# Performance work log

Hardware: AMD Instinct MI355X
Metric: run time of the kernel (lower is better)

Reference implementation:

```python
import jax, jax.numpy as jnp
import numpy as np

NUM_USERS = 100000
NUM_ITEMS = 50000
EMB_DIM = 128
NUM_LAYERS = 3
NUM_EDGES = 2000000
BATCH = 8192
REG = 1e-4


def setup_inputs() -> dict:
    key = jax.random.key(0)
    ks = jax.random.split(key, 8)
    N = NUM_USERS + NUM_ITEMS
    user_emb = jax.random.normal(ks[0], (NUM_USERS, EMB_DIM), dtype=jnp.float32) * 0.01
    item_emb = jax.random.normal(ks[1], (NUM_ITEMS, EMB_DIM), dtype=jnp.float32) * 0.01
    edge_row = jax.random.randint(ks[2], (NUM_EDGES,), 0, N, dtype=jnp.int32)
    edge_col = jax.random.randint(ks[3], (NUM_EDGES,), 0, N, dtype=jnp.int32)
    # symmetric-normalized adjacency values are small positives
    edge_val = jax.random.uniform(ks[4], (NUM_EDGES,), dtype=jnp.float32) * 0.1
    user = jax.random.randint(ks[5], (BATCH,), 0, NUM_USERS, dtype=jnp.int32)
    pos = jax.random.randint(ks[6], (BATCH,), 0, NUM_ITEMS, dtype=jnp.int32)
    neg = jax.random.randint(ks[7], (BATCH,), 0, NUM_ITEMS, dtype=jnp.int32)
    return {"user_emb": user_emb, "item_emb": item_emb,
            "edge_row": edge_row, "edge_col": edge_col, "edge_val": edge_val,
            "user": user, "pos": pos, "neg": neg}


def _lightgcn_embedding(user_emb, item_emb, edge_row, edge_col, edge_val):
    N = user_emb.shape[0] + item_emb.shape[0]
    emb = jnp.concatenate([user_emb, item_emb], axis=0)  # [N, D]
    acc = emb
    for _ in range(NUM_LAYERS):
        # SpMM: out[r] += val * emb[c] for each edge (r, c)
        msg = emb[edge_col] * edge_val[:, None]  # [E, D]
        emb = jax.ops.segment_sum(msg, edge_row, num_segments=N)
        acc = acc + emb
    light = acc / jnp.float32(NUM_LAYERS + 1)  # mean over layer outputs
    return light[:NUM_USERS], light[NUM_USERS:]


def reference(user_emb, item_emb, edge_row, edge_col, edge_val, user, pos, neg):
    u_all, i_all = _lightgcn_embedding(user_emb, item_emb, edge_row, edge_col, edge_val)
    u_lat = u_all[user]          # [B, D]
    pos_lat = i_all[pos]
    neg_lat = i_all[neg]
    pos_score = jnp.sum(u_lat * pos_lat, axis=1)
    neg_score = jnp.sum(u_lat * neg_lat, axis=1)
    # L1 regularization on ego (layer-0) embeddings, scalar broadcast onto batch loss
    reg_loss = REG * (jnp.sum(jnp.abs(user_emb[user]))
                      + jnp.sum(jnp.abs(item_emb[pos]))
                      + jnp.sum(jnp.abs(item_emb[neg])))
    batch_loss = jax.nn.softplus(neg_score - pos_score) + reg_loss
    return batch_loss
```

## Files before the change

kernel.cpp:

```cpp
#include <hip/hip_runtime.h>
#include <hip/hip_bf16.h>

#define EMB_D 128
#define BSH 9
#define MAXBUCK 512
#define CHUNKP 2048

typedef float f32x2 __attribute__((ext_vector_type(2)));

__device__ __forceinline__ float bf16_raw_to_f(unsigned short h) {
    return __uint_as_float(((unsigned int)h) << 16);
}
__device__ __forceinline__ float sane(float v) {
    return (v == v && fabsf(v) < 256.0f) ? v : 0.0f;
}
__device__ __forceinline__ float load_f(const void* p, int isf32, size_t idx) {
    return isf32 ? ((const float*)p)[idx]
                 : bf16_raw_to_f(((const unsigned short*)p)[idx]);
}

__device__ __forceinline__ f32x2 cvt2_fp8(unsigned int w) {
    f32x2 r;
    asm("v_cvt_pk_f32_fp8 %0, %1" : "=v"(r) : "v"(w));
    return r;
}
__device__ __forceinline__ unsigned int enc2_fp8(float a, float b) {
    unsigned int r;
    asm("v_cvt_pk_fp8_f32 %0, %1, %2" : "=v"(r) : "v"(a), "v"(b));
    return r & 0xFFFFu;
}
__device__ __forceinline__ unsigned int fp8x4_enc(float a, float b, float c, float d) {
    return enc2_fp8(a, b) | (enc2_fp8(c, d) << 16);
}
__device__ __forceinline__ float fp8_dec_byte(unsigned int b) {
    return cvt2_fp8(b & 0xFFu).x;
}

__global__ void k_detect(const unsigned short* __restrict__ ue,
                         const unsigned short* __restrict__ ie,
                         const unsigned short* __restrict__ ev,
                         int* __restrict__ flags) {
    int a = blockIdx.x;
    const unsigned short* p = (a == 0) ? ue : (a == 1) ? ie : ev;
    int lane = threadIdx.x;
    int cnt = 0;
    #pragma unroll
    for (int k = 0; k < 16; ++k) {
        float v = bf16_raw_to_f(p[k * 64 + lane]);
        if (!(fabsf(v) < 1.0f)) cnt++;
    }
    #pragma unroll
    for (int off = 32; off > 0; off >>= 1)
        cnt += __shfl_down(cnt, off, 64);
    if (lane == 0) flags[a] = (cnt > 64) ? 1 : 0;
}

__global__ __launch_bounds__(256) void k_build_emb8(
        const void* __restrict__ ue, const void* __restrict__ ie,
        const int* __restrict__ flags,
        unsigned char* __restrict__ T, float* __restrict__ S,
        int NU, int N) {
    int gid = blockIdx.x * blockDim.x + threadIdx.x;
    int row = gid >> 5;
    if (row >= N) return;
    int l = gid & 31;
    const void* src; long r; int f;
    if (row < NU) { src = ue; r = row;      f = flags[0]; }
    else          { src = ie; r = row - NU; f = flags[1]; }
    float v0, v1, v2, v3;
    if (f) {
        float4 t = ((const float4*)src)[r * 32 + l];
        v0 = sane(t.x); v1 = sane(t.y); v2 = sane(t.z); v3 = sane(t.w);
    } else {
        ushort4 t = ((const ushort4*)src)[r * 32 + l];
        v0 = sane(bf16_raw_to_f(t.x)); v1 = sane(bf16_raw_to_f(t.y));
        v2 = sane(bf16_raw_to_f(t.z)); v3 = sane(bf16_raw_to_f(t.w));
    }
    float m = fmaxf(fmaxf(fabsf(v0), fabsf(v1)), fmaxf(fabsf(v2), fabsf(v3)));
    #pragma unroll
    for (int off = 1; off < 32; off <<= 1)
        m = fmaxf(m, __shfl_xor(m, off, 64));
    float enc = (m > 0.0f) ? 448.0f / m : 0.0f;
    ((unsigned int*)T)[(size_t)row * 32 + l] =
        fp8x4_enc(v0 * enc, v1 * enc, v2 * enc, v3 * enc);
    if (l == 0) S[row] = (m > 0.0f) ? m * (1.0f / 448.0f) : 0.0f;
}

__global__ void k_zero_flags(int* __restrict__ f, int words, float* __restrict__ reg) {
    int i = blockIdx.x * blockDim.x + threadIdx.x;
    if (i < words) f[i] = 0;
    if (i == 0) reg[0] = 0.0f;
}

__global__ void k_mark_batch(const int* __restrict__ user, const int* __restrict__ pos,
                             const int* __restrict__ neg,
                             const void* __restrict__ ue, const void* __restrict__ ie,
                             const int* __restrict__ flags, int NU, int NI,
                             unsigned char* __restrict__ flag3,
                             unsigned char* __restrict__ flag2,
                             float* __restrict__ regp) {
    __shared__ float sred[2];
    int b = blockIdx.x;
    int d = threadIdx.x;
    int ui = min(max(user[b], 0), NU - 1);
    int pi = min(max(pos[b],  0), NI - 1);
    int ni = min(max(neg[b],  0), NI - 1);
    if (d == 0) {
        flag3[ui] = 1; flag3[NU + pi] = 1; flag3[NU + ni] = 1;
        flag2[ui] = 1; flag2[NU + pi] = 1; flag2[NU + ni] = 1;
    }
    int f0 = flags[0], f1 = flags[1];
    float u = sane(load_f(ue, f0, (size_t)ui * EMB_D + d));
    float p = sane(load_f(ie, f1, (size_t)pi * EMB_D + d));
    float n = sane(load_f(ie, f1, (size_t)ni * EMB_D + d));
    float s = fabsf(u) + fabsf(p) + fabsf(n);
    #pragma unroll
    for (int off = 32; off > 0; off >>= 1)
        s += __shfl_down(s, off, 64);
    if ((d & 63) == 0) sred[d >> 6] = s;
    __syncthreads();
    if (d == 0) regp[b] = sred[0] + sred[1];
}

__global__ void k_reduce_reg(const float* __restrict__ regp, float* __restrict__ reg, int B) {
    __shared__ float ss[256];
    int t = threadIdx.x;
    float s = 0.0f;
    for (int i = t; i < B; i += 256) s += regp[i];
    ss[t] = s;
    __syncthreads();
    for (int off = 128; off > 0; off >>= 1) {
        if (t < off) ss[t] += ss[t + off];
        __syncthreads();
    }
    if (t == 0) reg[0] = ss[0];
}


__global__ __launch_bounds__(256) void k_part_count(
        const int* __restrict__ erow, const int* __restrict__ ecol,
        const unsigned char* __restrict__ flag3, unsigned char* __restrict__ flag2,
        int* __restrict__ bcnt, int E, int N, int nbuck, int NB) {
    __shared__ int lh[MAXBUCK];
    int b = blockIdx.x, t = threadIdx.x;
    for (int i = t; i < MAXBUCK; i += 256) lh[i] = 0;
    __syncthreads();
    int beg = b * CHUNKP;
    int cnt = min(CHUNKP, E - beg);
    for (int p = t; p < cnt; p += 256) {
        int e = beg + p;
        int r = min(max(erow[e], 0), N - 1);
        atomicAdd(&lh[r >> BSH], 1);
        if (flag3[r]) {
            int c = min(max(ecol[e], 0), N - 1);
            flag2[c] = 1;
        }
    }
    __syncthreads();
    for (int i = t; i < nbuck; i += 256) bcnt[(long)i * NB + b] = lh[i];
}

__global__ void k_gscan1(const int* __restrict__ a, int* __restrict__ bsums, int L) {
    __shared__ int ss[256];
    int t = threadIdx.x;
    int base = blockIdx.x * 1024 + t * 4;
    int s = 0;
    #pragma unroll
    for (int j = 0; j < 4; ++j) {
        int idx = base + j;
        if (idx < L) s += a[idx];
    }
    ss[t] = s;
    __syncthreads();
    for (int off = 128; off > 0; off >>= 1) {
        if (t < off) ss[t] += ss[t + off];
        __syncthreads();
    }
    if (t == 0) bsums[blockIdx.x] = ss[0];
}

__global__ void k_gscan2(const int* __restrict__ bsums, int* __restrict__ boffs,
                         int nb, int* __restrict__ rowptrN) {
    __shared__ int ss[256];
    int t = threadIdx.x;
    int base = t * 4;
    int c[4];
    int s = 0;
    #pragma unroll
    for (int j = 0; j < 4; ++j) {
        c[j] = (base + j < nb) ? bsums[base + j] : 0;
        s += c[j];
    }
    ss[t] = s;
    __syncthreads();
    for (int off = 1; off < 256; off <<= 1) {
        int v = (t >= off) ? ss[t - off] : 0;
        __syncthreads();
        ss[t] += v;
        __syncthreads();
    }
    int run = ss[t] - s;
    #pragma unroll
    for (int j = 0; j < 4; ++j) {
        if (base + j < nb) boffs[base + j] = run;
        run += c[j];
    }
    if (t == 255) *rowptrN = ss[255];
}

__global__ void k_gscan3(int* __restrict__ a, const int* __restrict__ boffs, int L) {
    __shared__ int ss[256];
    int t = threadIdx.x;
    int base = blockIdx.x * 1024 + t * 4;
    int c[4];
    int s = 0;
    #pragma unroll
    for (int j = 0; j < 4; ++j) {
        int idx = base + j;
        c[j] = (idx < L) ? a[idx] : 0;
        s += c[j];
    }
    ss[t] = s;
    __syncthreads();
    for (int off = 1; off < 256; off <<= 1) {
        int v = (t >= off) ? ss[t - off] : 0;
        __syncthreads();
        ss[t] += v;
        __syncthreads();
    }
    int run = boffs[blockIdx.x] + ss[t] - s;
    #pragma unroll
    for (int j = 0; j < 4; ++j) {
        int idx = base + j;
        if (idx < L) a[idx] = run;
        run += c[j];
    }
}

__global__ __launch_bounds__(256) void k_part_scatter(
        const int* __restrict__ erow, const int* __restrict__ ecol,
        const void* __restrict__ eval, const int* __restrict__ flags,
        const int* __restrict__ boff,
        unsigned int* __restrict__ part_cv, unsigned short* __restrict__ part_r,
        int E, int N, int nbuck, int NB) {
    __shared__ uint2 lrec[CHUNKP];
    __shared__ unsigned short lidx[CHUNKP];
    __shared__ int hist[MAXBUCK];
    __shared__ int bstart[MAXBUCK];
    __shared__ int ss[256];
    int b = blockIdx.x, t = threadIdx.x;
    int beg = b * CHUNKP;
    int cnt = min(CHUNKP, E - beg);
    for (int i = t; i < MAXBUCK; i += 256) hist[i] = 0;
    __syncthreads();
    int f2 = flags[2];
    for (int p = t; p < cnt; p += 256) {
        int e = beg + p;
        int r = min(max(erow[e], 0), N - 1);
        int c = min(max(ecol[e], 0), N - 1);
        float v = sane(load_f(eval, f2, e));
        if (v < 0.0f) v = 0.0f;
        unsigned int u = __float_as_uint(v);
        unsigned int vb = ((u + 0x10000u) >> 17) & 0x3FFFu;
        lrec[p] = make_uint2((unsigned int)r, ((unsigned int)c << 14) | vb);
        atomicAdd(&hist[r >> BSH], 1);
    }
    __syncthreads();
    int c0 = hist[2 * t], c1 = hist[2 * t + 1];
    int s = c0 + c1;
    ss[t] = s;
    __syncthreads();
    for (int off = 1; off < 256; off <<= 1) {
        int v = (t >= off) ? ss[t - off] : 0;
        __syncthreads();
        ss[t] += v;
        __syncthreads();
    }
    int eb = ss[t] - s;
    bstart[2 * t] = eb;
    bstart[2 * t + 1] = eb + c0;
    hist[2 * t] = eb;
    hist[2 * t + 1] = eb + c0;
    __syncthreads();
    for (int p = t; p < cnt; p += 256) {
        int bin = (int)(lrec[p].x >> BSH);
        int pos = atomicAdd(&hist[bin], 1);
        lidx[pos] = (unsigned short)p;
    }
    __syncthreads();
    for (int i = t; i < nbuck; i += 256)
        hist[i] = boff[(long)i * NB + b] - bstart[i];
    __syncthreads();
    for (int p = t; p < cnt; p += 256) {
        uint2 rec = lrec[lidx[p]];
        int bin = (int)(rec.x >> BSH);
        int o = hist[bin] + p;
        part_cv[o] = rec.y;
        part_r[o] = (unsigned short)(rec.x & 511u);
    }
}

__global__ __launch_bounds__(256) void k_build_csr(
        const unsigned int* __restrict__ part_cv,
        const unsigned short* __restrict__ part_r,
        const int* __restrict__ boff,
        int* __restrict__ row_ptr, unsigned int* __restrict__ sedge,
        int E, int N, int NB, int nbuck) {
    __shared__ int rcnt[256];
    __shared__ int rcur[256];
    __shared__ int ss[256];
    __shared__ int slow;
    int blk = blockIdx.x, t = threadIdx.x;
    int bin = blk >> 1, half = blk & 1;
    int base = boff[(long)bin * NB];
    int next = (bin + 1 < nbuck) ? boff[(long)(bin + 1) * NB] : E;
    int cnt = next - base;
    int r0 = bin << BSH;
    int rlo = half << 8;
    int nrows = min(256, max(0, min(512, N - r0) - rlo));
    rcnt[t] = 0;
    if (t == 0) slow = 0;
    __syncthreads();
    int lowc = 0;
    for (int i = t; i < cnt; i += 256) {
        int pr = part_r[base + i];
        int lp = pr - rlo;
        if (lp >= 0 && lp < 256) atomicAdd(&rcnt[lp], 1);
        else if (pr < rlo) lowc++;
    }
    #pragma unroll
    for (int off = 32; off > 0; off >>= 1)
        lowc += __shfl_down(lowc, off, 64);
    if ((t & 63) == 0 && lowc) atomicAdd(&slow, lowc);
    __syncthreads();
    int c = rcnt[t];
    ss[t] = c;
    __syncthreads();
    for (int off = 1; off < 256; off <<= 1) {
        int v = (t >= off) ? ss[t - off] : 0;
        __syncthreads();
        ss[t] += v;
        __syncthreads();
    }
    int st = ss[t] - c + slow;
    rcur[t] = st;
    __syncthreads();
    if (t < nrows) row_ptr[r0 + rlo + t] = base + st;
    for (int i = t; i < cnt; i += 256) {
        int pr = part_r[base + i];
        int lp = pr - rlo;
        if (lp >= 0 && lp < 256) {
            int pos = atomicAdd(&rcur[lp], 1);
            sedge[base + pos] = part_cv[base + i];
        }
    }
}

__global__ __launch_bounds__(1024, 8) void k_spmm_csr8(
        const unsigned char* __restrict__ T, const float* __restrict__ S,
        unsigned char* __restrict__ Td, float* __restrict__ Sd,
        const int* __restrict__ row_ptr, const unsigned int* __restrict__ sedge,
        int N, const unsigned char* __restrict__ skipf, int use_skip) {
    int row = blockIdx.x * (blockDim.x >> 6) + (threadIdx.x >> 6);
    if (row >= N) return;
    if (use_skip && skipf[row] == 0) return;
    int lane = threadIdx.x & 63;
    int ph = lane >> 4;
    int sl = lane & 15;
    int beg = row_ptr[row], end = row_ptr[row + 1];
    float a[8];
    #pragma unroll
    for (int j = 0; j < 8; ++j) a[j] = 0.0f;
    int i = beg + ph;
    for (; i + 4 < end; i += 8) {
        unsigned int se0 = sedge[i];
        unsigned int se1 = sedge[i + 4];
        unsigned int c0 = se0 >> 14, c1 = se1 >> 14;
        uint2 h0 = ((const uint2*)(T + (size_t)c0 * EMB_D))[sl];
        uint2 h1 = ((const uint2*)(T + (size_t)c1 * EMB_D))[sl];
        float vs0 = __uint_as_float((se0 & 0x3FFFu) << 17) * S[c0];
        float vs1 = __uint_as_float((se1 & 0x3FFFu) << 17) * S[c1];
        f32x2 d;
        d = cvt2_fp8(h0.x);       a[0] += vs0 * d.x; a[1] += vs0 * d.y;
        d = cvt2_fp8(h0.x >> 16); a[2] += vs0 * d.x; a[3] += vs0 * d.y;
        d = cvt2_fp8(h0.y);       a[4] += vs0 * d.x; a[5] += vs0 * d.y;
        d = cvt2_fp8(h0.y >> 16); a[6] += vs0 * d.x; a[7] += vs0 * d.y;
        d = cvt2_fp8(h1.x);       a[0] += vs1 * d.x; a[1] += vs1 * d.y;
        d = cvt2_fp8(h1.x >> 16); a[2] += vs1 * d.x; a[3] += vs1 * d.y;
        d = cvt2_fp8(h1.y);       a[4] += vs1 * d.x; a[5] += vs1 * d.y;
        d = cvt2_fp8(h1.y >> 16); a[6] += vs1 * d.x; a[7] += vs1 * d.y;
    }
    if (i < end) {
        unsigned int se = sedge[i];
        unsigned int c = se >> 14;
        uint2 h = ((const uint2*)(T + (size_t)c * EMB_D))[sl];
        float vs = __uint_as_float((se & 0x3FFFu) << 17) * S[c];
        f32x2 d;
        d = cvt2_fp8(h.x);       a[0] += vs * d.x; a[1] += vs * d.y;
        d = cvt2_fp8(h.x >> 16); a[2] += vs * d.x; a[3] += vs * d.y;
        d = cvt2_fp8(h.y);       a[4] += vs * d.x; a[5] += vs * d.y;
        d = cvt2_fp8(h.y >> 16); a[6] += vs * d.x; a[7] += vs * d.y;
    }
    #pragma unroll
    for (int j = 0; j < 8; ++j) {
        a[j] += __shfl_xor(a[j], 16, 64);
        a[j] += __shfl_xor(a[j], 32, 64);
    }
    float m = fmaxf(fmaxf(fmaxf(fabsf(a[0]), fabsf(a[1])), fmaxf(fabsf(a[2]), fabsf(a[3]))),
                    fmaxf(fmaxf(fabsf(a[4]), fabsf(a[5])), fmaxf(fabsf(a[6]), fabsf(a[7]))));
    m = fmaxf(m, __shfl_xor(m, 1, 64));
    m = fmaxf(m, __shfl_xor(m, 2, 64));
    m = fmaxf(m, __shfl_xor(m, 4, 64));
    m = fmaxf(m, __shfl_xor(m, 8, 64));
    if (ph == 0) {
        float enc = (m > 0.0f) ? 448.0f / m : 0.0f;
        uint2 w;
        w.x = fp8x4_enc(a[0] * enc, a[1] * enc, a[2] * enc, a[3] * enc);
        w.y = fp8x4_enc(a[4] * enc, a[5] * enc, a[6] * enc, a[7] * enc);
        ((uint2*)(Td + (size_t)row * EMB_D))[sl] = w;
        if (lane == 0) Sd[row] = (m > 0.0f) ? m * (1.0f / 448.0f) : 0.0f;
    }
}

__global__ void k_gather_final(
        const void* __restrict__ ue, const void* __restrict__ ie,
        const int* __restrict__ flags,
        const int* __restrict__ user, const int* __restrict__ pos,
        const int* __restrict__ neg, int NU, int NI,
        const unsigned char* __restrict__ T1, const float* __restrict__ S1,
        const unsigned char* __restrict__ T2, const float* __restrict__ S2,
        const unsigned char* __restrict__ T3, const float* __restrict__ S3,
        const float* __restrict__ reg, float* __restrict__ out) {
    __shared__ float sps[2], sns[2];
    int b = blockIdx.x;
    int d = threadIdx.x;
    int ui = min(max(user[b], 0), NU - 1);
    int pi = min(max(pos[b],  0), NI - 1);
    int ni = min(max(neg[b],  0), NI - 1);
    size_t ru = (size_t)ui;
    size_t rp = (size_t)NU + pi;
    size_t rn = (size_t)NU + ni;
    int f0 = flags[0], f1 = flags[1];
    float u = sane(load_f(ue, f0, ru * EMB_D + d))
            + fp8_dec_byte(T1[ru * EMB_D + d]) * S1[ru]
            + fp8_dec_byte(T2[ru * EMB_D + d]) * S2[ru]
            + fp8_dec_byte(T3[ru * EMB_D + d]) * S3[ru];
    float p = sane(load_f(ie, f1, (size_t)pi * EMB_D + d))
            + fp8_dec_byte(T1[rp * EMB_D + d]) * S1[rp]
            + fp8_dec_byte(T2[rp * EMB_D + d]) * S2[rp]
            + fp8_dec_byte(T3[rp * EMB_D + d]) * S3[rp];
    float n = sane(load_f(ie, f1, (size_t)ni * EMB_D + d))
            + fp8_dec_byte(T1[rn * EMB_D + d]) * S1[rn]
            + fp8_dec_byte(T2[rn * EMB_D + d]) * S2[rn]
            + fp8_dec_byte(T3[rn * EMB_D + d]) * S3[rn];
    float ps = u * p, ns = u * n;
    #pragma unroll
    for (int off = 32; off > 0; off >>= 1) {
        ps += __shfl_down(ps, off, 64);
        ns += __shfl_down(ns, off, 64);
    }
    if ((d & 63) == 0) { sps[d >> 6] = ps; sns[d >> 6] = ns; }
    __syncthreads();
    if (d == 0) {
        float x = ((sns[0] + sns[1]) - (sps[0] + sps[1])) * 0.0625f;
        float sp = fmaxf(x, 0.0f) + log1pf(expf(-fabsf(x)));
        out[b] = sp + 1e-4f * reg[0];
    }
}

extern "C" void kernel_launch(void* const* d_in, const int* in_sizes, int n_in,
                              void* d_out, int out_size, void* d_ws, size_t ws_size,
                              hipStream_t stream) {
    const void* ue   = d_in[0];
    const void* ie   = d_in[1];
    const int*  erow = (const int*)d_in[2];
    const int*  ecol = (const int*)d_in[3];
    const void* ev   = d_in[4];
    const int*  user = (const int*)d_in[5];
    const int*  pos  = (const int*)d_in[6];
    const int*  neg  = (const int*)d_in[7];

    int NU = in_sizes[0] / EMB_D;
    int NI = in_sizes[1] / EMB_D;
    int N  = NU + NI;
    int E  = in_sizes[2];
    int B  = in_sizes[5];

    int nbuck = (N + ((1 << BSH) - 1)) >> BSH;
    int NBp   = (E + CHUNKP - 1) / CHUNKP;
    int L     = nbuck * NBp;
    int nbL   = (L + 1023) / 1024;

    size_t T8   = (size_t)N * EMB_D;
    size_t SC   = (((size_t)N * sizeof(float)) + 15) & ~15ull;
    size_t NI4  = ((size_t)(N + 1) * sizeof(int) + 15) & ~15ull;
    size_t L4   = ((size_t)L * sizeof(int) + 15) & ~15ull;
    size_t E2   = (((size_t)E * 2) + 15) & ~15ull;
    size_t Npad = ((size_t)N + 15) & ~15ull;
    char* w = (char*)d_ws;
    int*   flags   = (int*)w;
    float* reg     = (float*)(w + 64);
    char*  q       = w + 256;
    float* regp    = (float*)q;             q += (size_t)B * sizeof(float);
    int*   row_ptr = (int*)q;               q += NI4;
    unsigned int*   part_cv = (unsigned int*)q;   q += (size_t)E * 4;
    unsigned short* part_r  = (unsigned short*)q; q += E2;
    int*   bcnt    = (int*)q;               q += L4;
    int*   bsums   = (int*)q;               q += 4096;
    int*   boffs   = (int*)q;               q += 4096;
    unsigned char* flag3 = (unsigned char*)q; q += Npad;
    unsigned char* flag2 = (unsigned char*)q; q += Npad;
    unsigned int* sedge = (unsigned int*)q; q += (size_t)E * 4;
    unsigned char* Ta = (unsigned char*)q;  q += T8;
    float*         Sa = (float*)q;          q += SC;
    unsigned char* T1 = (unsigned char*)q;  q += T8;
    float*         S1 = (float*)q;          q += SC;
    unsigned char* T2 = (unsigned char*)q;  q += T8;
    float*         S2 = (float*)q;          q += SC;
    unsigned char* T3 = (unsigned char*)q;  q += T8;
    float*         S3 = (float*)q;

    const int thr = 256;
    float* out = (float*)d_out;

    k_detect<<<3, 64, 0, stream>>>((const unsigned short*)ue, (const unsigned short*)ie,
                                   (const unsigned short*)ev, flags);
    int fwords = (int)((2 * Npad) / 4);
    k_zero_flags<<<(fwords + thr - 1) / thr, thr, 0, stream>>>((int*)flag3, fwords, reg);
    k_mark_batch<<<B, EMB_D, 0, stream>>>(user, pos, neg, ue, ie, flags, NU, NI,
                                          flag3, flag2, regp);
    k_reduce_reg<<<1, 256, 0, stream>>>(regp, reg, B);
    k_build_emb8<<<(N * 32 + thr - 1) / thr, thr, 0, stream>>>(ue, ie, flags, Ta, Sa, NU, N);

    k_part_count<<<NBp, 256, 0, stream>>>(erow, ecol, flag3, flag2, bcnt, E, N, nbuck, NBp);
    k_gscan1<<<nbL, 256, 0, stream>>>(bcnt, bsums, L);
    k_gscan2<<<1, 256, 0, stream>>>(bsums, boffs, nbL, row_ptr + N);
    k_gscan3<<<nbL, 256, 0, stream>>>(bcnt, boffs, L);
    k_part_scatter<<<NBp, 256, 0, stream>>>(erow, ecol, ev, flags, bcnt,
                                            part_cv, part_r, E, N, nbuck, NBp);
    k_build_csr<<<2 * nbuck, 256, 0, stream>>>(part_cv, part_r, bcnt, row_ptr, sedge,
                                               E, N, NBp, nbuck);

    const int sthr = 1024;
    int rows_per_block = sthr / 64;
    int sgrid = (N + rows_per_block - 1) / rows_per_block;

    k_spmm_csr8<<<sgrid, sthr, 0, stream>>>(Ta, Sa, T1, S1, row_ptr, sedge, N, flag2, 0);
    k_spmm_csr8<<<sgrid, sthr, 0, stream>>>(T1, S1, T2, S2, row_ptr, sedge, N, flag2, 1);
    k_spmm_csr8<<<sgrid, sthr, 0, stream>>>(T2, S2, T3, S3, row_ptr, sedge, N, flag3, 1);

    k_gather_final<<<B, EMB_D, 0, stream>>>(ue, ie, flags, user, pos, neg, NU, NI,
                                            T1, S1, T2, S2, T3, S3, reg, out);
}
```

Before: 460.5 us.

## Fuse setup kernels, replace multi-pass bucket scan with atomic cursors, shrink SpMM blocks

Merges format detection, flag zeroing and bucket-counter clearing into one setup kernel, and merges the FP8 embedding build with the batch marking and regularizer partial sums into one prep kernel. The per-chunk bucket count matrix and its three-kernel global scan are replaced by global atomic bucket counts, a single-block scan (which also reduces the regularizer) and atomic cursors for scatter offsets. SpMM launches now use 256-thread blocks without launch bounds. The aim is fewer launches and a smaller scan. In exchange the order of edges inside each bucket depends on scheduling, and the global atomics add some contention.

After: 476.7 us. 3.5% more time.

```diff
diff --git a/kernel.cpp b/kernel.cpp
--- a/kernel.cpp
+++ b/kernel.cpp
@@ -36,111 +36,101 @@
     return cvt2_fp8(b & 0xFFu).x;
 }
 
-__global__ void k_detect(const unsigned short* __restrict__ ue,
-                         const unsigned short* __restrict__ ie,
-                         const unsigned short* __restrict__ ev,
-                         int* __restrict__ flags) {
-    int a = blockIdx.x;
-    const unsigned short* p = (a == 0) ? ue : (a == 1) ? ie : ev;
-    int lane = threadIdx.x;
-    int cnt = 0;
-    #pragma unroll
-    for (int k = 0; k < 16; ++k) {
-        float v = bf16_raw_to_f(p[k * 64 + lane]);
-        if (!(fabsf(v) < 1.0f)) cnt++;
-    }
-    #pragma unroll
-    for (int off = 32; off > 0; off >>= 1)
-        cnt += __shfl_down(cnt, off, 64);
-    if (lane == 0) flags[a] = (cnt > 64) ? 1 : 0;
-}
-
-__global__ __launch_bounds__(256) void k_build_emb8(
+__global__ void k_setup(const unsigned short* __restrict__ ue,
+                        const unsigned short* __restrict__ ie,
+                        const unsigned short* __restrict__ ev,
+                        int* __restrict__ flags,
+                        int* __restrict__ fzero, int fwords,
+                        int* __restrict__ bucket_cnt) {
+    int gid = blockIdx.x * blockDim.x + threadIdx.x;
+    for (int i = gid; i < fwords; i += gridDim.x * blockDim.x) fzero[i] = 0;
+    if (gid < MAXBUCK) bucket_cnt[gid] = 0;
+    if (blockIdx.x < 3 && threadIdx.x < 64) {
+        int a = blockIdx.x;
+        const unsigned short* p = (a == 0) ? ue : (a == 1) ? ie : ev;
+        int lane = threadIdx.x;
+        int cnt = 0;
+        #pragma unroll
+        for (int k = 0; k < 16; ++k) {
+            float v = bf16_raw_to_f(p[k * 64 + lane]);
+            if (!(fabsf(v) < 1.0f)) cnt++;
+        }
+        #pragma unroll
+        for (int off = 32; off > 0; off >>= 1)
+            cnt += __shfl_down(cnt, off, 64);
+        if (lane == 0) flags[a] = (cnt > 64) ? 1 : 0;
+    }
+}
+
+__global__ __launch_bounds__(256) void k_prep(
         const void* __restrict__ ue, const void* __restrict__ ie,
         const int* __restrict__ flags,
         unsigned char* __restrict__ T, float* __restrict__ S,
-        int NU, int N) {
-    int gid = blockIdx.x * blockDim.x + threadIdx.x;
-    int row = gid >> 5;
-    if (row >= N) return;
-    int l = gid & 31;
-    const void* src; long r; int f;
-    if (row < NU) { src = ue; r = row;      f = flags[0]; }
-    else          { src = ie; r = row - NU; f = flags[1]; }
-    float v0, v1, v2, v3;
-    if (f) {
-        float4 t = ((const float4*)src)[r * 32 + l];
-        v0 = sane(t.x); v1 = sane(t.y); v2 = sane(t.z); v3 = sane(t.w);
+        int NU, int NI, int N,
+        const int* __restrict__ user, const int* __restrict__ pos,
+        const int* __restrict__ neg, int B,
+        unsigned char* __restrict__ flag3, unsigned char* __restrict__ flag2,
+        float* __restrict__ regp, int GE) {
+    __shared__ float sredw[4];
+    if (blockIdx.x < GE) {
+        int gid = blockIdx.x * 256 + threadIdx.x;
+        int row = gid >> 5;
+        if (row >= N) return;
+        int l = gid & 31;
+        const void* src; long r; int f;
+        if (row < NU) { src = ue; r = row;      f = flags[0]; }
+        else          { src = ie; r = row - NU; f = flags[1]; }
+        float v0, v1, v2, v3;
+        if (f) {
+            float4 t = ((const float4*)src)[r * 32 + l];
+            v0 = sane(t.x); v1 = sane(t.y); v2 = sane(t.z); v3 = sane(t.w);
+        } else {
+            ushort4 t = ((const ushort4*)src)[r * 32 + l];
+            v0 = sane(bf16_raw_to_f(t.x)); v1 = sane(bf16_raw_to_f(t.y));
+            v2 = sane(bf16_raw_to_f(t.z)); v3 = sane(bf16_raw_to_f(t.w));
+        }
+        float m = fmaxf(fmaxf(fabsf(v0), fabsf(v1)), fmaxf(fabsf(v2), fabsf(v3)));
+        #pragma unroll
+        for (int off = 1; off < 32; off <<= 1)
+            m = fmaxf(m, __shfl_xor(m, off, 64));
+        float enc = (m > 0.0f) ? 448.0f / m : 0.0f;
+        ((unsigned int*)T)[(size_t)row * 32 + l] =
+            fp8x4_enc(v0 * enc, v1 * enc, v2 * enc, v3 * enc);
+        if (l == 0) S[row] = (m > 0.0f) ? m * (1.0f / 448.0f) : 0.0f;
     } else {
-        ushort4 t = ((const ushort4*)src)[r * 32 + l];
-        v0 = sane(bf16_raw_to_f(t.x)); v1 = sane(bf16_raw_to_f(t.y));
-        v2 = sane(bf16_raw_to_f(t.z)); v3 = sane(bf16_raw_to_f(t.w));
-    }
-    float m = fmaxf(fmaxf(fabsf(v0), fabsf(v1)), fmaxf(fabsf(v2), fabsf(v3)));
-    #pragma unroll
-    for (int off = 1; off < 32; off <<= 1)
-        m = fmaxf(m, __shfl_xor(m, off, 64));
-    float enc = (m > 0.0f) ? 448.0f / m : 0.0f;
-    ((unsigned int*)T)[(size_t)row * 32 + l] =
-        fp8x4_enc(v0 * enc, v1 * enc, v2 * enc, v3 * enc);
-    if (l == 0) S[row] = (m > 0.0f) ? m * (1.0f / 448.0f) : 0.0f;
-}
-
-__global__ void k_zero_flags(int* __restrict__ f, int words, float* __restrict__ reg) {
-    int i = blockIdx.x * blockDim.x + threadIdx.x;
-    if (i < words) f[i] = 0;
-    if (i == 0) reg[0] = 0.0f;
-}
-
-__global__ void k_mark_batch(const int* __restrict__ user, const int* __restrict__ pos,
-                             const int* __restrict__ neg,
-                             const void* __restrict__ ue, const void* __restrict__ ie,
-                             const int* __restrict__ flags, int NU, int NI,
-                             unsigned char* __restrict__ flag3,
-                             unsigned char* __restrict__ flag2,
-                             float* __restrict__ regp) {
-    __shared__ float sred[2];
-    int b = blockIdx.x;
-    int d = threadIdx.x;
-    int ui = min(max(user[b], 0), NU - 1);
-    int pi = min(max(pos[b],  0), NI - 1);
-    int ni = min(max(neg[b],  0), NI - 1);
-    if (d == 0) {
-        flag3[ui] = 1; flag3[NU + pi] = 1; flag3[NU + ni] = 1;
-        flag2[ui] = 1; flag2[NU + pi] = 1; flag2[NU + ni] = 1;
-    }
-    int f0 = flags[0], f1 = flags[1];
-    float u = sane(load_f(ue, f0, (size_t)ui * EMB_D + d));
-    float p = sane(load_f(ie, f1, (size_t)pi * EMB_D + d));
-    float n = sane(load_f(ie, f1, (size_t)ni * EMB_D + d));
-    float s = fabsf(u) + fabsf(p) + fabsf(n);
-    #pragma unroll
-    for (int off = 32; off > 0; off >>= 1)
-        s += __shfl_down(s, off, 64);
-    if ((d & 63) == 0) sred[d >> 6] = s;
-    __syncthreads();
-    if (d == 0) regp[b] = sred[0] + sred[1];
-}
-
-__global__ void k_reduce_reg(const float* __restrict__ regp, float* __restrict__ reg, int B) {
-    __shared__ float ss[256];
-    int t = threadIdx.x;
-    float s = 0.0f;
-    for (int i = t; i < B; i += 256) s += regp[i];
-    ss[t] = s;
-    __syncthreads();
-    for (int off = 128; off > 0; off >>= 1) {
-        if (t < off) ss[t] += ss[t + off];
-        __syncthreads();
-    }
-    if (t == 0) reg[0] = ss[0];
+        int t = threadIdx.x;
+        int half = t >> 7;
+        int d = t & 127;
+        int b = (blockIdx.x - GE) * 2 + half;
+        float s = 0.0f;
+        if (b < B) {
+            int ui = min(max(user[b], 0), NU - 1);
+            int pi = min(max(pos[b],  0), NI - 1);
+            int ni = min(max(neg[b],  0), NI - 1);
+            if (d == 0) {
+                flag3[ui] = 1; flag3[NU + pi] = 1; flag3[NU + ni] = 1;
+                flag2[ui] = 1; flag2[NU + pi] = 1; flag2[NU + ni] = 1;
+            }
+            int f0 = flags[0], f1 = flags[1];
+            float u = sane(load_f(ue, f0, (size_t)ui * EMB_D + d));
+            float p = sane(load_f(ie, f1, (size_t)pi * EMB_D + d));
+            float n = sane(load_f(ie, f1, (size_t)ni * EMB_D + d));
+            s = fabsf(u) + fabsf(p) + fabsf(n);
+        }
+        #pragma unroll
+        for (int off = 32; off > 0; off >>= 1)
+            s += __shfl_down(s, off, 64);
+        if ((t & 63) == 0) sredw[t >> 6] = s;
+        __syncthreads();
+        if (b < B && d == 0) regp[b] = sredw[half * 2] + sredw[half * 2 + 1];
+    }
 }
 
 
 __global__ __launch_bounds__(256) void k_part_count(
         const int* __restrict__ erow, const int* __restrict__ ecol,
         const unsigned char* __restrict__ flag3, unsigned char* __restrict__ flag2,
-        int* __restrict__ bcnt, int E, int N, int nbuck, int NB) {
+        int* __restrict__ bucket_cnt, int E, int N, int nbuck) {
     __shared__ int lh[MAXBUCK];
     int b = blockIdx.x, t = threadIdx.x;
     for (int i = t; i < MAXBUCK; i += 256) lh[i] = 0;
@@ -157,40 +147,23 @@
         }
     }
     __syncthreads();
-    for (int i = t; i < nbuck; i += 256) bcnt[(long)i * NB + b] = lh[i];
-}
-
-__global__ void k_gscan1(const int* __restrict__ a, int* __restrict__ bsums, int L) {
+    for (int i = t; i < nbuck; i += 256) {
+        int c = lh[i];
+        if (c) atomicAdd(&bucket_cnt[i], c);
+    }
+}
+
+__global__ void k_scan_reg(const int* __restrict__ bucket_cnt,
+                           int* __restrict__ bucket_base, int* __restrict__ cursor,
+                           int* __restrict__ rowptrN,
+                           const float* __restrict__ regp, float* __restrict__ reg,
+                           int nbuck, int B) {
     __shared__ int ss[256];
+    __shared__ float fs[256];
     int t = threadIdx.x;
-    int base = blockIdx.x * 1024 + t * 4;
-    int s = 0;
-    #pragma unroll
-    for (int j = 0; j < 4; ++j) {
-        int idx = base + j;
-        if (idx < L) s += a[idx];
-    }
-    ss[t] = s;
-    __syncthreads();
-    for (int off = 128; off > 0; off >>= 1) {
-        if (t < off) ss[t] += ss[t + off];
-        __syncthreads();
-    }
-    if (t == 0) bsums[blockIdx.x] = ss[0];
-}
-
-__global__ void k_gscan2(const int* __restrict__ bsums, int* __restrict__ boffs,
-                         int nb, int* __restrict__ rowptrN) {
-    __shared__ int ss[256];
-    int t = threadIdx.x;
-    int base = t * 4;
-    int c[4];
-    int s = 0;
-    #pragma unroll
-    for (int j = 0; j < 4; ++j) {
-        c[j] = (base + j < nb) ? bsums[base + j] : 0;
-        s += c[j];
-    }
+    int c0 = (2 * t     < nbuck) ? bucket_cnt[2 * t]     : 0;
+    int c1 = (2 * t + 1 < nbuck) ? bucket_cnt[2 * t + 1] : 0;
+    int s = c0 + c1;
     ss[t] = s;
     __syncthreads();
     for (int off = 1; off < 256; off <<= 1) {
@@ -199,50 +172,29 @@
         ss[t] += v;
         __syncthreads();
     }
-    int run = ss[t] - s;
-    #pragma unroll
-    for (int j = 0; j < 4; ++j) {
-        if (base + j < nb) boffs[base + j] = run;
-        run += c[j];
-    }
+    int eb = ss[t] - s;
+    if (2 * t < nbuck) { bucket_base[2 * t] = eb; cursor[2 * t] = eb; }
+    if (2 * t == nbuck) bucket_base[nbuck] = eb;
+    if (2 * t + 1 < nbuck) { bucket_base[2 * t + 1] = eb + c0; cursor[2 * t + 1] = eb + c0; }
+    if (2 * t + 1 == nbuck) bucket_base[nbuck] = eb + c0;
     if (t == 255) *rowptrN = ss[255];
-}
-
-__global__ void k_gscan3(int* __restrict__ a, const int* __restrict__ boffs, int L) {
-    __shared__ int ss[256];
-    int t = threadIdx.x;
-    int base = blockIdx.x * 1024 + t * 4;
-    int c[4];
-    int s = 0;
-    #pragma unroll
-    for (int j = 0; j < 4; ++j) {
-        int idx = base + j;
-        c[j] = (idx < L) ? a[idx] : 0;
-        s += c[j];
-    }
-    ss[t] = s;
-    __syncthreads();
-    for (int off = 1; off < 256; off <<= 1) {
-        int v = (t >= off) ? ss[t - off] : 0;
-        __syncthreads();
-        ss[t] += v;
-        __syncthreads();
-    }
-    int run = boffs[blockIdx.x] + ss[t] - s;
-    #pragma unroll
-    for (int j = 0; j < 4; ++j) {
-        int idx = base + j;
-        if (idx < L) a[idx] = run;
-        run += c[j];
-    }
+    float f = 0.0f;
+    for (int i = t; i < B; i += 256) f += regp[i];
+    fs[t] = f;
+    __syncthreads();
+    for (int off = 128; off > 0; off >>= 1) {
+        if (t < off) fs[t] += fs[t + off];
+        __syncthreads();
+    }
+    if (t == 0) reg[0] = fs[0];
 }
 
 __global__ __launch_bounds__(256) void k_part_scatter(
         const int* __restrict__ erow, const int* __restrict__ ecol,
         const void* __restrict__ eval, const int* __restrict__ flags,
-        const int* __restrict__ boff,
+        int* __restrict__ cursor,
         unsigned int* __restrict__ part_cv, unsigned short* __restrict__ part_r,
-        int E, int N, int nbuck, int NB) {
+        int E, int N, int nbuck) {
     __shared__ uint2 lrec[CHUNKP];
     __shared__ unsigned short lidx[CHUNKP];
     __shared__ int hist[MAXBUCK];
@@ -288,8 +240,8 @@
         lidx[pos] = (unsigned short)p;
     }
     __syncthreads();
-    for (int i = t; i < nbuck; i += 256)
-        hist[i] = boff[(long)i * NB + b] - bstart[i];
+    if (c0 > 0) hist[2 * t]     = atomicAdd(&cursor[2 * t],     c0) - bstart[2 * t];
+    if (c1 > 0) hist[2 * t + 1] = atomicAdd(&cursor[2 * t + 1], c1) - bstart[2 * t + 1];
     __syncthreads();
     for (int p = t; p < cnt; p += 256) {
         uint2 rec = lrec[lidx[p]];
@@ -303,17 +255,17 @@
 __global__ __launch_bounds__(256) void k_build_csr(
         const unsigned int* __restrict__ part_cv,
         const unsigned short* __restrict__ part_r,
-        const int* __restrict__ boff,
+        const int* __restrict__ bucket_base,
         int* __restrict__ row_ptr, unsigned int* __restrict__ sedge,
-        int E, int N, int NB, int nbuck) {
+        int E, int N, int nbuck) {
     __shared__ int rcnt[256];
     __shared__ int rcur[256];
     __shared__ int ss[256];
     __shared__ int slow;
     int blk = blockIdx.x, t = threadIdx.x;
     int bin = blk >> 1, half = blk & 1;
-    int base = boff[(long)bin * NB];
-    int next = (bin + 1 < nbuck) ? boff[(long)(bin + 1) * NB] : E;
+    int base = bucket_base[bin];
+    int next = bucket_base[bin + 1];
     int cnt = next - base;
     int r0 = bin << BSH;
     int rlo = half << 8;
@@ -356,7 +308,7 @@
     }
 }
 
-__global__ __launch_bounds__(1024, 8) void k_spmm_csr8(
+__global__ void k_spmm_csr8(
         const unsigned char* __restrict__ T, const float* __restrict__ S,
         unsigned char* __restrict__ Td, float* __restrict__ Sd,
         const int* __restrict__ row_ptr, const unsigned int* __restrict__ sedge,
@@ -488,13 +440,10 @@
 
     int nbuck = (N + ((1 << BSH) - 1)) >> BSH;
     int NBp   = (E + CHUNKP - 1) / CHUNKP;
-    int L     = nbuck * NBp;
-    int nbL   = (L + 1023) / 1024;
 
     size_t T8   = (size_t)N * EMB_D;
     size_t SC   = (((size_t)N * sizeof(float)) + 15) & ~15ull;
     size_t NI4  = ((size_t)(N + 1) * sizeof(int) + 15) & ~15ull;
-    size_t L4   = ((size_t)L * sizeof(int) + 15) & ~15ull;
     size_t E2   = (((size_t)E * 2) + 15) & ~15ull;
     size_t Npad = ((size_t)N + 15) & ~15ull;
     char* w = (char*)d_ws;
@@ -505,9 +454,9 @@
     int*   row_ptr = (int*)q;               q += NI4;
     unsigned int*   part_cv = (unsigned int*)q;   q += (size_t)E * 4;
     unsigned short* part_r  = (unsigned short*)q; q += E2;
-    int*   bcnt    = (int*)q;               q += L4;
-    int*   bsums   = (int*)q;               q += 4096;
-    int*   boffs   = (int*)q;               q += 4096;
+    int*   bucket_cnt  = (int*)q;           q += MAXBUCK * sizeof(int);
+    int*   bucket_base = (int*)q;           q += (MAXBUCK + 8) * sizeof(int);
+    int*   cursor      = (int*)q;           q += MAXBUCK * sizeof(int);
     unsigned char* flag3 = (unsigned char*)q; q += Npad;
     unsigned char* flag2 = (unsigned char*)q; q += Npad;
     unsigned int* sedge = (unsigned int*)q; q += (size_t)E * 4;
@@ -523,31 +472,33 @@
     const int thr = 256;
     float* out = (float*)d_out;
 
-    k_detect<<<3, 64, 0, stream>>>((const unsigned short*)ue, (const unsigned short*)ie,
-                                   (const unsigned short*)ev, flags);
     int fwords = (int)((2 * Npad) / 4);
-    k_zero_flags<<<(fwords + thr - 1) / thr, thr, 0, stream>>>((int*)flag3, fwords, reg);
-    k_mark_batch<<<B, EMB_D, 0, stream>>>(user, pos, neg, ue, ie, flags, NU, NI,
-                                          flag3, flag2, regp);
-    k_reduce_reg<<<1, 256, 0, stream>>>(regp, reg, B);
-    k_build_emb8<<<(N * 32 + thr - 1) / thr, thr, 0, stream>>>(ue, ie, flags, Ta, Sa, NU, N);
-
-    k_part_count<<<NBp, 256, 0, stream>>>(erow, ecol, flag3, flag2, bcnt, E, N, nbuck, NBp);
-    k_gscan1<<<nbL, 256, 0, stream>>>(bcnt, bsums, L);
-    k_gscan2<<<1, 256, 0, stream>>>(bsums, boffs, nbL, row_ptr + N);
-    k_gscan3<<<nbL, 256, 0, stream>>>(bcnt, boffs, L);
-    k_part_scatter<<<NBp, 256, 0, stream>>>(erow, ecol, ev, flags, bcnt,
-                                            part_cv, part_r, E, N, nbuck, NBp);
-    k_build_csr<<<2 * nbuck, 256, 0, stream>>>(part_cv, part_r, bcnt, row_ptr, sedge,
-                                               E, N, NBp, nbuck);
-
-    const int sthr = 1024;
-    int rows_per_block = sthr / 64;
+    int zgrid = (fwords + thr - 1) / thr;
+    if (zgrid < 4) zgrid = 4;
+    k_setup<<<zgrid, thr, 0, stream>>>((const unsigned short*)ue,
+                                       (const unsigned short*)ie,
+                                       (const unsigned short*)ev,
+                                       flags, (int*)flag3, fwords, bucket_cnt);
+
+    int GE = (N * 32 + thr - 1) / thr;
+    int MBlk = (B + 1) / 2;
+    k_prep<<<GE + MBlk, thr, 0, stream>>>(ue, ie, flags, Ta, Sa, NU, NI, N,
+                                          user, pos, neg, B, flag3, flag2, regp, GE);
+
+    k_part_count<<<NBp, 256, 0, stream>>>(erow, ecol, flag3, flag2, bucket_cnt,
+                                          E, N, nbuck);
+    k_scan_reg<<<1, 256, 0, stream>>>(bucket_cnt, bucket_base, cursor,
+                                      row_ptr + N, regp, reg, nbuck, B);
+    k_part_scatter<<<NBp, 256, 0, stream>>>(erow, ecol, ev, flags, cursor,
+                                            part_cv, part_r, E, N, nbuck);
+    k_build_csr<<<2 * nbuck, 256, 0, stream>>>(part_cv, part_r, bucket_base,
+                                               row_ptr, sedge, E, N, nbuck);
+
+    int rows_per_block = thr / 64;
     int sgrid = (N + rows_per_block - 1) / rows_per_block;
-
-    k_spmm_csr8<<<sgrid, sthr, 0, stream>>>(Ta, Sa, T1, S1, row_ptr, sedge, N, flag2, 0);
-    k_spmm_csr8<<<sgrid, sthr, 0, stream>>>(T1, S1, T2, S2, row_ptr, sedge, N, flag2, 1);
-    k_spmm_csr8<<<sgrid, sthr, 0, stream>>>(T2, S2, T3, S3, row_ptr, sedge, N, flag3, 1);
+    k_spmm_csr8<<<sgrid, thr, 0, stream>>>(Ta, Sa, T1, S1, row_ptr, sedge, N, flag2, 0);
+    k_spmm_csr8<<<sgrid, thr, 0, stream>>>(T1, S1, T2, S2, row_ptr, sedge, N, flag2, 1);
+    k_spmm_csr8<<<sgrid, thr, 0, stream>>>(T2, S2, T3, S3, row_ptr, sedge, N, flag3, 1);
 
     k_gather_final<<<B, EMB_D, 0, stream>>>(ue, ie, flags, user, pos, neg, NU, NI,
                                             T1, S1, T2, S2, T3, S3, reg, out);
```
